# Performance work log

Hardware: AMD Instinct MI355X
Metric: run time of the kernel (lower is better)

The kernel has to match this reference:

```python
import jax, jax.numpy as jnp
import numpy as np

B, NNZ = 2048, 8
CAT_V, HVEC_V = 10000, 50000
SYN, SEM = 128, 256
HIDDEN, OUT = 1024, 10000


def setup_inputs() -> dict:
    key = jax.random.key(0)
    ks = jax.random.split(key, 12)
    d_onehot = jax.nn.one_hot(jax.random.randint(ks[0], (B,), 0, 7), 7, dtype=jnp.float32)
    cat_b_ix = jax.random.randint(ks[1], (B,), 0, CAT_V)
    hvb_ix = jax.random.randint(ks[2], (B, NNZ), 0, HVEC_V)
    hvf_ix = jax.random.randint(ks[3], (B, NNZ), 0, HVEC_V)
    hvb_top = jax.random.normal(ks[4], (B, SEM), dtype=jnp.float32)
    hvf_top = jax.random.normal(ks[5], (B, SEM), dtype=jnp.float32)
    cat_embeds = jax.random.normal(ks[6], (CAT_V, SYN), dtype=jnp.float32) * 0.02
    hvec_embeds = jax.random.normal(ks[7], (HVEC_V, SEM), dtype=jnp.float32) * 0.02
    in_dim = 7 + SYN + 2 * SEM
    W1 = jax.random.normal(ks[8], (HIDDEN, in_dim), dtype=jnp.float32) / np.sqrt(in_dim)
    b1 = jnp.zeros((HIDDEN,), dtype=jnp.float32)
    W2 = jax.random.normal(ks[9], (OUT, HIDDEN), dtype=jnp.float32) / np.sqrt(HIDDEN)
    b2 = jnp.zeros((OUT,), dtype=jnp.float32)
    return {"d_onehot": d_onehot, "cat_b_ix": cat_b_ix, "hvb_ix": hvb_ix,
            "hvf_ix": hvf_ix, "hvb_top": hvb_top, "hvf_top": hvf_top,
            "cat_embeds": cat_embeds, "hvec_embeds": hvec_embeds,
            "W1": W1, "b1": b1, "W2": W2, "b2": b2}


def _multi_hot(ix, vocab):
    # set-to-1 semantics: duplicates within a row still yield 1 (matches torch loop)
    rows = jnp.arange(ix.shape[0])[:, None]
    return jnp.zeros((ix.shape[0], vocab), dtype=jnp.float32).at[rows, ix].set(1.0)


def reference(d_onehot, cat_b_ix, hvb_ix, hvf_ix, hvb_top, hvf_top,
              cat_embeds, hvec_embeds, W1, b1, W2, b2):
    cat_b_embed = cat_embeds[cat_b_ix]                      # (B, SYN)
    hvb_mat = _multi_hot(hvb_ix, hvec_embeds.shape[0])      # (B, HVEC_V)
    hvf_mat = _multi_hot(hvf_ix, hvec_embeds.shape[0])
    hvb_embed = hvb_mat @ hvec_embeds + hvb_top             # (B, SEM)
    hvf_embed = hvf_mat @ hvec_embeds + hvf_top
    x = jnp.concatenate([cat_b_embed, hvb_embed, hvf_embed, d_onehot], axis=1)
    x = jax.nn.relu(x @ W1.T + b1)
    x = x @ W2.T + b2
    return jax.nn.log_softmax(x, axis=1)
```

## Files before the change

kernel.cpp:

```cpp
#include <hip/hip_runtime.h>

#define B_      2048
#define SYN     128
#define SEM     256
#define IN_DIM  647
#define K1      704
#define HIDDEN  1024
#define OUT_N   10000
#define NNZ     8

typedef __bf16 bf16x8 __attribute__((ext_vector_type(8)));
typedef float  f32x4  __attribute__((ext_vector_type(4)));
typedef __attribute__((address_space(3))) const unsigned short* lds_cp;

__device__ __forceinline__ unsigned short f2b(float v) {
    __bf16 b = (__bf16)v;
    return __builtin_bit_cast(unsigned short, b);
}

#define NB_W1 2816
#define NB_W2 5000
__global__ __launch_bounds__(256) void prep(
    const float* __restrict__ W1,  unsigned short* __restrict__ W1b,
    const float* __restrict__ W2,  unsigned short* __restrict__ W2b,
    const float* __restrict__ d_onehot,
    const int*   __restrict__ cat_ix,
    const int*   __restrict__ hvb_ix,
    const int*   __restrict__ hvf_ix,
    const float* __restrict__ hvb_top,
    const float* __restrict__ hvf_top,
    const float* __restrict__ cat_embeds,
    const float* __restrict__ hvec_embeds,
    unsigned short* __restrict__ xb)
{
    const int bb = blockIdx.x, t = threadIdx.x;
    if (bb < NB_W1) {
        int idx = bb * 256 + t;
        int r = idx / K1, c = idx - r * K1;
        W1b[idx] = f2b(c < IN_DIM ? W1[r * IN_DIM + c] : 0.f);
        return;
    }
    if (bb < NB_W1 + NB_W2) {
        size_t i = (size_t)(bb - NB_W1) * 256 + t;
        const float4* src = (const float4*)(W2 + i * 8);
        float4 a = src[0], b = src[1];
        ushort u[8] = { f2b(a.x), f2b(a.y), f2b(a.z), f2b(a.w),
                        f2b(b.x), f2b(b.y), f2b(b.z), f2b(b.w) };
        *(uint4*)(W2b + i * 8) = *(const uint4*)u;
        return;
    }
    const int b = bb - (NB_W1 + NB_W2);
    unsigned short* xrow = xb + (size_t)b * K1;
    if (t < SYN) {
        int c = cat_ix[b];
        xrow[t] = f2b(cat_embeds[(size_t)c * SYN + t]);
    }
    {
        int ix[NNZ];
        #pragma unroll
        for (int j = 0; j < NNZ; ++j) ix[j] = hvb_ix[b * NNZ + j];
        float s = hvb_top[(size_t)b * SEM + t];
        #pragma unroll
        for (int j = 0; j < NNZ; ++j) {
            bool dup = false;
            for (int k2 = 0; k2 < j; ++k2) dup = dup || (ix[j] == ix[k2]);
            if (!dup) s += hvec_embeds[(size_t)ix[j] * SEM + t];
        }
        xrow[SYN + t] = f2b(s);
    }
    {
        int ix[NNZ];
        #pragma unroll
        for (int j = 0; j < NNZ; ++j) ix[j] = hvf_ix[b * NNZ + j];
        float s = hvf_top[(size_t)b * SEM + t];
        #pragma unroll
        for (int j = 0; j < NNZ; ++j) {
            bool dup = false;
            for (int k2 = 0; k2 < j; ++k2) dup = dup || (ix[j] == ix[k2]);
            if (!dup) s += hvec_embeds[(size_t)ix[j] * SEM + t];
        }
        xrow[SYN + SEM + t] = f2b(s);
    }
    if (t < 7)       xrow[640 + t] = f2b(d_onehot[b * 7 + t]);
    else if (t < 64) xrow[640 + t] = 0;
}

template<int NI, int MODE>
__global__ __launch_bounds__(256) void gemm_rt(
    const unsigned short* __restrict__ A,
    const unsigned short* __restrict__ Bm,
    const float* __restrict__ bias,
    void* __restrict__ outp,
    int K, int nt, int ncols, int nbm1, int nm)
{
    constexpr int BN    = 32 * NI;
    constexpr int NB_CH = NI / 2;
    __shared__ __align__(16) unsigned short lds_a[4][128 * 32];
    __shared__ __align__(16) unsigned short lds_b[4][BN * 32];

    const int tid = threadIdx.x;
    const int wv = tid >> 6, ln = tid & 63;
    const int wr = wv >> 1, wc = wv & 1;
    const int lr = ln & 15, lh = ln >> 4;

    const int g   = gridDim.x;
    const int nw  = (blockIdx.x & 7) * (g >> 3) + (blockIdx.x >> 3);
    const int mt  = nw % nm, ntile = nw / nm;
    const int m0  = mt * 128, n0 = ntile * BN;

    const unsigned short* srcA[2];
    const unsigned short* srcB[NB_CH];
    #pragma unroll
    for (int i = 0; i < 2; ++i) {
        int c = tid + i * 256;
        int row = c >> 2, colL = (((c & 3) ^ ((c >> 3) & 3)) << 3);
        srcA[i] = A + (size_t)(m0 + row) * K + colL;
    }
    #pragma unroll
    for (int j = 0; j < NB_CH; ++j) {
        int c = tid + j * 256;
        int row = c >> 2, colL = (((c & 3) ^ ((c >> 3) & 3)) << 3);
        int gr = n0 + row; if (gr > nbm1) gr = nbm1;
        srcB[j] = Bm + (size_t)gr * K + colL;
    }

    auto stage = [&](int buf, int kt) {
        #pragma unroll
        for (int i = 0; i < 2; ++i)
            __builtin_amdgcn_global_load_lds(
                (__attribute__((address_space(1))) const void*)(srcA[i] + kt),
                (__attribute__((address_space(3))) void*)&lds_a[buf][(tid + i * 256) * 8], 16, 0, 0);
        #pragma unroll
        for (int j = 0; j < NB_CH; ++j)
            __builtin_amdgcn_global_load_lds(
                (__attribute__((address_space(1))) const void*)(srcB[j] + kt),
                (__attribute__((address_space(3))) void*)&lds_b[buf][(tid + j * 256) * 8], 16, 0, 0);
    };

    int a_off[4], b_off[NI];
    #pragma unroll
    for (int mi = 0; mi < 4; ++mi) {
        int row = wr * 64 + mi * 16 + lr;
        a_off[mi] = (row * 64 + lh * 16) ^ (((row >> 1) & 3) << 4);
    }
    #pragma unroll
    for (int ni = 0; ni < NI; ++ni) {
        int row = wc * 16 * NI + ni * 16 + lr;
        b_off[ni] = (row * 64 + lh * 16) ^ (((row >> 1) & 3) << 4);
    }

    f32x4 acc[4][NI];
    {
        f32x4 z = {0.f, 0.f, 0.f, 0.f};
        #pragma unroll
        for (int i = 0; i < 4; ++i)
            #pragma unroll
            for (int j = 0; j < NI; ++j) acc[i][j] = z;
    }

    auto frag_read = [&](bf16x8 (&af)[4], bf16x8 (&bfv)[NI], int buf) {
        lds_cp pa = (lds_cp)&lds_a[buf][0];
        lds_cp pb = (lds_cp)&lds_b[buf][0];
        #pragma unroll
        for (int mi = 0; mi < 4; ++mi) {
            unsigned ad = (unsigned)(unsigned long long)pa + a_off[mi];
            asm volatile("ds_read_b128 %0, %1" : "=v"(af[mi]) : "v"(ad));
        }
        #pragma unroll
        for (int ni = 0; ni < NI; ++ni) {
            unsigned ad = (unsigned)(unsigned long long)pb + b_off[ni];
            asm volatile("ds_read_b128 %0, %1" : "=v"(bfv[ni]) : "v"(ad));
        }
    };
    auto do_mfma = [&](bf16x8 (&af)[4], bf16x8 (&bfv)[NI]) {
        #pragma unroll
        for (int mi = 0; mi < 4; ++mi)
            #pragma unroll
            for (int ni = 0; ni < NI; ++ni)
                acc[mi][ni] = __builtin_amdgcn_mfma_f32_16x16x32_bf16(af[mi], bfv[ni], acc[mi][ni], 0, 0, 0);
    };
    auto do_part = [&](bf16x8 (&rA)[4], bf16x8 (&rB)[NI],
                       bf16x8 (&mA)[4], bf16x8 (&mB)[NI], int p) {
        frag_read(rA, rB, (p + 1) & 3);
        int tp = p + 3; if (tp > nt - 1) tp = nt - 1;
        stage((p + 3) & 3, tp * 32);
        if constexpr (NI == 4) asm volatile("s_waitcnt lgkmcnt(8)" ::: "memory");
        else                   asm volatile("s_waitcnt lgkmcnt(6)" ::: "memory");
        __builtin_amdgcn_sched_barrier(0);
        __builtin_amdgcn_s_setprio(1);
        do_mfma(mA, mB);
        __builtin_amdgcn_s_setprio(0);
        if constexpr (NI == 4) asm volatile("s_waitcnt vmcnt(4)" ::: "memory");
        else                   asm volatile("s_waitcnt vmcnt(3)" ::: "memory");
        __builtin_amdgcn_s_barrier();
    };

    stage(0, 0);
    stage(1, 32);
    stage(2, 64);
    if constexpr (NI == 4) asm volatile("s_waitcnt vmcnt(4)" ::: "memory");
    else                   asm volatile("s_waitcnt vmcnt(3)" ::: "memory");
    __builtin_amdgcn_s_barrier();

    bf16x8 afX[4], bfX[NI], afY[4], bfY[NI];
    frag_read(afX, bfX, 0);

    for (int t = 0; t < nt; t += 2) {
        do_part(afY, bfY, afX, bfX, t);
        do_part(afX, bfX, afY, bfY, t + 1);
    }

    #pragma unroll
    for (int mi = 0; mi < 4; ++mi) {
        int row = m0 + wr * 64 + mi * 16 + lh * 4;
        #pragma unroll
        for (int ni = 0; ni < NI; ++ni) {
            int col = n0 + wc * 16 * NI + ni * 16 + lr;
            if (col < ncols) {
                float bb = bias[col];
                if (MODE == 0) {
                    unsigned short* H = (unsigned short*)outp;
                    #pragma unroll
                    for (int r = 0; r < 4; ++r)
                        H[(size_t)(row + r) * ncols + col] = f2b(fmaxf(acc[mi][ni][r] + bb, 0.f));
                } else if (MODE == 1) {
                    unsigned short* H = (unsigned short*)outp;
                    #pragma unroll
                    for (int r = 0; r < 4; ++r)
                        H[(size_t)(row + r) * ncols + col] = f2b(acc[mi][ni][r] + bb);
                } else {
                    float* O = (float*)outp;
                    #pragma unroll
                    for (int r = 0; r < 4; ++r)
                        O[(size_t)(row + r) * ncols + col] = acc[mi][ni][r] + bb;
                }
            }
        }
    }
}

__global__ __launch_bounds__(256) void lsm_b(const unsigned short* __restrict__ lg,
                                             float* __restrict__ out) {
    __shared__ __align__(16) float rowbuf[OUT_N];
    __shared__ float red[8];
    const int t = threadIdx.x, wv = t >> 6, ln = t & 63;
    const unsigned short* l = lg + (size_t)blockIdx.x * OUT_N;
    float* o = out + (size_t)blockIdx.x * OUT_N;

    float mx = -3.4e38f;
    for (int i = t; i < OUT_N / 8; i += 256) {
        uint4 v = ((const uint4*)l)[i];
        float f[8];
        unsigned w[4] = {v.x, v.y, v.z, v.w};
        #pragma unroll
        for (int j = 0; j < 4; ++j) {
            f[2*j]   = __builtin_bit_cast(float, w[j] << 16);
            f[2*j+1] = __builtin_bit_cast(float, w[j] & 0xffff0000u);
        }
        #pragma unroll
        for (int j = 0; j < 8; ++j) {
            rowbuf[i * 8 + j] = f[j];
            mx = fmaxf(mx, f[j]);
        }
    }
    #pragma unroll
    for (int off = 32; off > 0; off >>= 1) mx = fmaxf(mx, __shfl_xor(mx, off, 64));
    if (ln == 0) red[wv] = mx;
    __syncthreads();
    float m4 = fmaxf(fmaxf(red[0], red[1]), fmaxf(red[2], red[3]));

    float s = 0.f;
    for (int i = t; i < OUT_N; i += 256) s += __expf(rowbuf[i] - m4);
    #pragma unroll
    for (int off = 32; off > 0; off >>= 1) s += __shfl_xor(s, off, 64);
    if (ln == 0) red[4 + wv] = s;
    __syncthreads();
    float lz = m4 + logf(red[4] + red[5] + red[6] + red[7]);

    for (int i = t; i < OUT_N / 4; i += 256) {
        float4 v = { rowbuf[i*4] - lz, rowbuf[i*4+1] - lz,
                     rowbuf[i*4+2] - lz, rowbuf[i*4+3] - lz };
        ((float4*)o)[i] = v;
    }
}

__global__ __launch_bounds__(256) void lsm_f(float* __restrict__ out) {
    __shared__ __align__(16) float rowbuf[OUT_N];
    __shared__ float red[8];
    const int t = threadIdx.x, wv = t >> 6, ln = t & 63;
    float* o = out + (size_t)blockIdx.x * OUT_N;

    float mx = -3.4e38f;
    for (int i = t; i < OUT_N / 4; i += 256) {
        float4 v = ((const float4*)o)[i];
        rowbuf[i*4] = v.x; rowbuf[i*4+1] = v.y; rowbuf[i*4+2] = v.z; rowbuf[i*4+3] = v.w;
        mx = fmaxf(fmaxf(mx, fmaxf(v.x, v.y)), fmaxf(v.z, v.w));
    }
    #pragma unroll
    for (int off = 32; off > 0; off >>= 1) mx = fmaxf(mx, __shfl_xor(mx, off, 64));
    if (ln == 0) red[wv] = mx;
    __syncthreads();
    float m4 = fmaxf(fmaxf(red[0], red[1]), fmaxf(red[2], red[3]));

    float s = 0.f;
    for (int i = t; i < OUT_N; i += 256) s += __expf(rowbuf[i] - m4);
    #pragma unroll
    for (int off = 32; off > 0; off >>= 1) s += __shfl_xor(s, off, 64);
    if (ln == 0) red[4 + wv] = s;
    __syncthreads();
    float lz = m4 + logf(red[4] + red[5] + red[6] + red[7]);

    for (int i = t; i < OUT_N / 4; i += 256) {
        float4 v = { rowbuf[i*4] - lz, rowbuf[i*4+1] - lz,
                     rowbuf[i*4+2] - lz, rowbuf[i*4+3] - lz };
        ((float4*)o)[i] = v;
    }
}

extern "C" void kernel_launch(void* const* d_in, const int* in_sizes, int n_in,
                              void* d_out, int out_size, void* d_ws, size_t ws_size,
                              hipStream_t stream) {
    const float* d_onehot    = (const float*)d_in[0];
    const int*   cat_ix      = (const int*)  d_in[1];
    const int*   hvb_ix      = (const int*)  d_in[2];
    const int*   hvf_ix      = (const int*)  d_in[3];
    const float* hvb_top     = (const float*)d_in[4];
    const float* hvf_top     = (const float*)d_in[5];
    const float* cat_embeds  = (const float*)d_in[6];
    const float* hvec_embeds = (const float*)d_in[7];
    const float* W1          = (const float*)d_in[8];
    const float* b1          = (const float*)d_in[9];
    const float* W2          = (const float*)d_in[10];
    const float* b2          = (const float*)d_in[11];
    float* out = (float*)d_out;

    unsigned short* xb  = (unsigned short*)d_ws;
    unsigned short* W1b = xb  + (size_t)B_ * K1;
    unsigned short* hB  = W1b + (size_t)HIDDEN * K1;
    unsigned short* W2b = hB  + (size_t)B_ * HIDDEN;
    unsigned short* lg  = W2b + (size_t)OUT_N * HIDDEN;
    const size_t need = ((size_t)B_*K1 + (size_t)HIDDEN*K1 + (size_t)B_*HIDDEN
                         + (size_t)OUT_N*HIDDEN + (size_t)B_*OUT_N) * 2;
    const bool bf16_logits = (ws_size >= need);

    prep<<<dim3(NB_W1 + NB_W2 + B_), dim3(256), 0, stream>>>(
        W1, W1b, W2, W2b, d_onehot, cat_ix, hvb_ix, hvf_ix,
        hvb_top, hvf_top, cat_embeds, hvec_embeds, xb);
    gemm_rt<2, 0><<<dim3(256), dim3(256), 0, stream>>>(
        xb, W1b, b1, (void*)hB, K1, K1 / 32, HIDDEN, HIDDEN - 1, 16);
    if (bf16_logits) {
        gemm_rt<4, 1><<<dim3(16 * 79), dim3(256), 0, stream>>>(
            hB, W2b, b2, (void*)lg, HIDDEN, HIDDEN / 32, OUT_N, OUT_N - 1, 16);
        lsm_b<<<dim3(B_), dim3(256), 0, stream>>>(lg, out);
    } else {
        gemm_rt<4, 2><<<dim3(16 * 79), dim3(256), 0, stream>>>(
            hB, W2b, b2, (void*)out, HIDDEN, HIDDEN / 32, OUT_N, OUT_N - 1, 16);
        lsm_f<<<dim3(B_), dim3(256), 0, stream>>>(out);
    }
}
```

Baseline: 116.3 us.

## Add 256x320-tile 4-stage pipelined GEMM for logits layer

Replaces the generic second GEMM (128-row tiles, 1264 blocks) with a dedicated 512-thread kernel using 256x320 tiles, giving exactly 256 blocks that cover 2048x10240 outputs. It keeps a 4-slot LDS ring filled with direct global-to-LDS loads, splits each k-step into two MFMA halves interleaved with staging, uses a swizzled LDS layout and raises wave priority around the MFMAs. The goal is to cut operand re-reads and tile-count overhead and to overlap loads with compute better. The cost is heavy register and LDS use (about 144KB LDS per block), and the last tile wastes columns past 10000.

```diff
diff --git a/kernel.cpp b/kernel.cpp
--- a/kernel.cpp
+++ b/kernel.cpp
@@ -223,17 +223,159 @@
                     #pragma unroll
                     for (int r = 0; r < 4; ++r)
                         H[(size_t)(row + r) * ncols + col] = f2b(fmaxf(acc[mi][ni][r] + bb, 0.f));
-                } else if (MODE == 1) {
-                    unsigned short* H = (unsigned short*)outp;
-                    #pragma unroll
-                    for (int r = 0; r < 4; ++r)
-                        H[(size_t)(row + r) * ncols + col] = f2b(acc[mi][ni][r] + bb);
                 } else {
                     float* O = (float*)outp;
                     #pragma unroll
                     for (int r = 0; r < 4; ++r)
                         O[(size_t)(row + r) * ncols + col] = acc[mi][ni][r] + bb;
                 }
+            }
+        }
+    }
+}
+
+__global__ __launch_bounds__(512, 2) void gemm2_320(
+    const unsigned short* __restrict__ A,
+    const unsigned short* __restrict__ Bm,
+    const float* __restrict__ bias,
+    unsigned short* __restrict__ H)
+{
+    __shared__ __align__(16) unsigned short lA[4][8192];
+    __shared__ __align__(16) unsigned short lB[4][10240];
+    const int tid = threadIdx.x;
+    const int wv = tid >> 6, ln = tid & 63;
+    const int wr = wv >> 2, wc = wv & 3;
+    const int lr = ln & 15, lh = ln >> 4;
+
+    const int nw = (blockIdx.x & 7) * 32 + (blockIdx.x >> 3);
+    const int m0 = (nw & 7) * 256;
+    const int n0 = (nw >> 3) * 320;
+
+    const unsigned short* srcA[2];
+    const unsigned short* srcB[2];
+    const unsigned short* srcB2;
+    #pragma unroll
+    for (int j = 0; j < 2; ++j) {
+        int c = j * 512 + tid;
+        int row = c >> 2, colL = (((c & 3) ^ ((c >> 3) & 3)) << 3);
+        srcA[j] = A + (size_t)(m0 + row) * HIDDEN + colL;
+        int gr = n0 + row; if (gr > OUT_N - 1) gr = OUT_N - 1;
+        srcB[j] = Bm + (size_t)gr * HIDDEN + colL;
+    }
+    const int c2 = 1024 + (wv & 3) * 64 + ln;
+    {
+        int row = c2 >> 2, colL = (((c2 & 3) ^ ((c2 >> 3) & 3)) << 3);
+        int gr = n0 + row; if (gr > OUT_N - 1) gr = OUT_N - 1;
+        srcB2 = Bm + (size_t)gr * HIDDEN + colL;
+    }
+
+    auto stageA = [&](int slot, int kt) {
+        #pragma unroll
+        for (int j = 0; j < 2; ++j)
+            __builtin_amdgcn_global_load_lds(
+                (__attribute__((address_space(1))) const void*)(srcA[j] + kt),
+                (__attribute__((address_space(3))) void*)&lA[slot][(j * 512 + tid) * 8], 16, 0, 0);
+    };
+    auto stageB = [&](int slot, int kt) {
+        #pragma unroll
+        for (int j = 0; j < 2; ++j)
+            __builtin_amdgcn_global_load_lds(
+                (__attribute__((address_space(1))) const void*)(srcB[j] + kt),
+                (__attribute__((address_space(3))) void*)&lB[slot][(j * 512 + tid) * 8], 16, 0, 0);
+        __builtin_amdgcn_global_load_lds(
+            (__attribute__((address_space(1))) const void*)(srcB2 + kt),
+            (__attribute__((address_space(3))) void*)&lB[slot][c2 * 8], 16, 0, 0);
+    };
+
+    int a_off[8], b_off[5];
+    #pragma unroll
+    for (int mi = 0; mi < 8; ++mi) {
+        int row = wr * 128 + mi * 16 + lr;
+        a_off[mi] = (row * 64 + lh * 16) ^ (((row >> 1) & 3) << 4);
+    }
+    #pragma unroll
+    for (int ni = 0; ni < 5; ++ni) {
+        int row = wc * 80 + ni * 16 + lr;
+        b_off[ni] = (row * 64 + lh * 16) ^ (((row >> 1) & 3) << 4);
+    }
+
+    f32x4 acc[8][5];
+    {
+        f32x4 z = {0.f, 0.f, 0.f, 0.f};
+        #pragma unroll
+        for (int i = 0; i < 8; ++i)
+            #pragma unroll
+            for (int j = 0; j < 5; ++j) acc[i][j] = z;
+    }
+
+    stageA(0, 0);  stageB(0, 0);
+    stageA(1, 32); stageB(1, 32);
+    stageA(2, 64); stageB(2, 64);
+    asm volatile("s_waitcnt vmcnt(10)" ::: "memory");
+    __builtin_amdgcn_s_barrier();
+
+    for (int t = 0; t < 32; ++t) {
+        const int slot = t & 3;
+        int tp = t + 3; if (tp > 31) tp = 31;
+        const int pslot = tp & 3;
+        lds_cp pA = (lds_cp)&lA[slot][0];
+        lds_cp pB = (lds_cp)&lB[slot][0];
+        bf16x8 af[4], bfv[5];
+
+        #pragma unroll
+        for (int ni = 0; ni < 5; ++ni) {
+            unsigned ad = (unsigned)(unsigned long long)pB + b_off[ni];
+            asm volatile("ds_read_b128 %0, %1" : "=v"(bfv[ni]) : "v"(ad));
+        }
+        #pragma unroll
+        for (int mi = 0; mi < 4; ++mi) {
+            unsigned ad = (unsigned)(unsigned long long)pA + a_off[mi];
+            asm volatile("ds_read_b128 %0, %1" : "=v"(af[mi]) : "v"(ad));
+        }
+        stageA(pslot, tp * 32);
+        __builtin_amdgcn_s_barrier();
+        asm volatile("s_waitcnt lgkmcnt(0)" ::: "memory");
+        __builtin_amdgcn_sched_barrier(0);
+        __builtin_amdgcn_s_setprio(1);
+        #pragma unroll
+        for (int mi = 0; mi < 4; ++mi)
+            #pragma unroll
+            for (int ni = 0; ni < 5; ++ni)
+                acc[mi][ni] = __builtin_amdgcn_mfma_f32_16x16x32_bf16(af[mi], bfv[ni], acc[mi][ni], 0, 0, 0);
+        __builtin_amdgcn_s_setprio(0);
+        __builtin_amdgcn_s_barrier();
+
+        #pragma unroll
+        for (int mi = 0; mi < 4; ++mi) {
+            unsigned ad = (unsigned)(unsigned long long)pA + a_off[4 + mi];
+            asm volatile("ds_read_b128 %0, %1" : "=v"(af[mi]) : "v"(ad));
+        }
+        stageB(pslot, tp * 32);
+        __builtin_amdgcn_s_barrier();
+        asm volatile("s_waitcnt lgkmcnt(0)" ::: "memory");
+        __builtin_amdgcn_sched_barrier(0);
+        __builtin_amdgcn_s_setprio(1);
+        #pragma unroll
+        for (int mi = 0; mi < 4; ++mi)
+            #pragma unroll
+            for (int ni = 0; ni < 5; ++ni)
+                acc[4 + mi][ni] = __builtin_amdgcn_mfma_f32_16x16x32_bf16(af[mi], bfv[ni], acc[4 + mi][ni], 0, 0, 0);
+        __builtin_amdgcn_s_setprio(0);
+        asm volatile("s_waitcnt vmcnt(10)" ::: "memory");
+        __builtin_amdgcn_s_barrier();
+    }
+
+    #pragma unroll
+    for (int mi = 0; mi < 8; ++mi) {
+        int row = m0 + wr * 128 + mi * 16 + lh * 4;
+        #pragma unroll
+        for (int ni = 0; ni < 5; ++ni) {
+            int col = n0 + wc * 80 + ni * 16 + lr;
+            if (col < OUT_N) {
+                float bb = bias[col];
+                #pragma unroll
+                for (int r = 0; r < 4; ++r)
+                    H[(size_t)(row + r) * OUT_N + col] = f2b(acc[mi][ni][r] + bb);
             }
         }
     }
@@ -349,8 +491,7 @@
     gemm_rt<2, 0><<<dim3(256), dim3(256), 0, stream>>>(
         xb, W1b, b1, (void*)hB, K1, K1 / 32, HIDDEN, HIDDEN - 1, 16);
     if (bf16_logits) {
-        gemm_rt<4, 1><<<dim3(16 * 79), dim3(256), 0, stream>>>(
-            hB, W2b, b2, (void*)lg, HIDDEN, HIDDEN / 32, OUT_N, OUT_N - 1, 16);
+        gemm2_320<<<dim3(256), dim3(512), 0, stream>>>(hB, W2b, b2, lg);
         lsm_b<<<dim3(B_), dim3(256), 0, stream>>>(lg, out);
     } else {
         gemm_rt<4, 2><<<dim3(16 * 79), dim3(256), 0, stream>>>(
```

After: 102.9 us. 11.5% less time.

## Widen output GEMM tile to 160 columns and simplify the prefetch pipeline

Applied to the files above, without the earlier changes.

The second GEMM moves from 128-wide to 160-wide N tiles (NI=5). The odd fifth B chunk is loaded by only half the threads, so the vmcnt waits are now per-wave. The main loop drops register-level fragment double buffering and the 3-deep prefetch in favour of a single-fragment loop with 2-deep LDS prefetch and a full lgkmcnt wait. Launch bounds now request 2 waves per SIMD, so occupancy rather than software pipelining is meant to hide latency. The grid of 1024 blocks includes a column of tiles lying fully beyond 10000 columns; those blocks do wasted work, and the simpler pipeline exposes LDS read latency.

```diff
diff --git a/kernel.cpp b/kernel.cpp
--- a/kernel.cpp
+++ b/kernel.cpp
@@ -85,16 +85,38 @@
     else if (t < 64) xrow[640 + t] = 0;
 }
 
+template<int NI> __device__ __forceinline__ void wait_vm(int wv) {
+    if constexpr (NI == 5) {
+        if (wv < 2) asm volatile("s_waitcnt vmcnt(5)" ::: "memory");
+        else        asm volatile("s_waitcnt vmcnt(4)" ::: "memory");
+    } else if constexpr (NI == 4) {
+        asm volatile("s_waitcnt vmcnt(4)" ::: "memory");
+    } else {
+        asm volatile("s_waitcnt vmcnt(3)" ::: "memory");
+    }
+}
+template<int NI> __device__ __forceinline__ void wait_vm2(int wv) {
+    if constexpr (NI == 5) {
+        if (wv < 2) asm volatile("s_waitcnt vmcnt(5)" ::: "memory");
+        else        asm volatile("s_waitcnt vmcnt(4)" ::: "memory");
+    } else if constexpr (NI == 4) {
+        asm volatile("s_waitcnt vmcnt(4)" ::: "memory");
+    } else {
+        asm volatile("s_waitcnt vmcnt(3)" ::: "memory");
+    }
+}
+
 template<int NI, int MODE>
-__global__ __launch_bounds__(256) void gemm_rt(
+__global__ __launch_bounds__(256, 2) void gemm_rt(
     const unsigned short* __restrict__ A,
     const unsigned short* __restrict__ Bm,
     const float* __restrict__ bias,
     void* __restrict__ outp,
     int K, int nt, int ncols, int nbm1, int nm)
 {
-    constexpr int BN    = 32 * NI;
-    constexpr int NB_CH = NI / 2;
+    constexpr int BN  = 32 * NI;
+    constexpr int BCH = NI / 2;
+    constexpr bool BX = (NI & 1);
     __shared__ __align__(16) unsigned short lds_a[4][128 * 32];
     __shared__ __align__(16) unsigned short lds_b[4][BN * 32];
 
@@ -109,7 +131,8 @@
     const int m0  = mt * 128, n0 = ntile * BN;
 
     const unsigned short* srcA[2];
-    const unsigned short* srcB[NB_CH];
+    const unsigned short* srcB[BCH];
+    const unsigned short* srcBx = nullptr;
     #pragma unroll
     for (int i = 0; i < 2; ++i) {
         int c = tid + i * 256;
@@ -117,12 +140,18 @@
         srcA[i] = A + (size_t)(m0 + row) * K + colL;
     }
     #pragma unroll
-    for (int j = 0; j < NB_CH; ++j) {
+    for (int j = 0; j < BCH; ++j) {
         int c = tid + j * 256;
         int row = c >> 2, colL = (((c & 3) ^ ((c >> 3) & 3)) << 3);
         int gr = n0 + row; if (gr > nbm1) gr = nbm1;
         srcB[j] = Bm + (size_t)gr * K + colL;
     }
+    if constexpr (BX) {
+        int c = tid + BCH * 256;
+        int row = c >> 2, colL = (((c & 3) ^ ((c >> 3) & 3)) << 3);
+        int gr = n0 + row; if (gr > nbm1) gr = nbm1;
+        srcBx = Bm + (size_t)gr * K + colL;
+    }
 
     auto stage = [&](int buf, int kt) {
         #pragma unroll
@@ -131,10 +160,16 @@
                 (__attribute__((address_space(1))) const void*)(srcA[i] + kt),
                 (__attribute__((address_space(3))) void*)&lds_a[buf][(tid + i * 256) * 8], 16, 0, 0);
         #pragma unroll
-        for (int j = 0; j < NB_CH; ++j)
+        for (int j = 0; j < BCH; ++j)
             __builtin_amdgcn_global_load_lds(
                 (__attribute__((address_space(1))) const void*)(srcB[j] + kt),
                 (__attribute__((address_space(3))) void*)&lds_b[buf][(tid + j * 256) * 8], 16, 0, 0);
+        if constexpr (BX) {
+            if (tid < 128)
+                __builtin_amdgcn_global_load_lds(
+                    (__attribute__((address_space(1))) const void*)(srcBx + kt),
+                    (__attribute__((address_space(3))) void*)&lds_b[buf][(tid + BCH * 256) * 8], 16, 0, 0);
+        }
     };
 
     int a_off[4], b_off[NI];
@@ -158,9 +193,18 @@
             for (int j = 0; j < NI; ++j) acc[i][j] = z;
     }
 
-    auto frag_read = [&](bf16x8 (&af)[4], bf16x8 (&bfv)[NI], int buf) {
-        lds_cp pa = (lds_cp)&lds_a[buf][0];
-        lds_cp pb = (lds_cp)&lds_b[buf][0];
+    stage(0, 0);
+    stage(1, 32);
+    wait_vm2<NI>(wv);
+    __builtin_amdgcn_s_barrier();
+
+    for (int t = 0; t < nt; ++t) {
+        const int slot = t & 3;
+        int tp = t + 2; if (tp > nt - 1) tp = nt - 1;
+
+        bf16x8 af[4], bfv[NI];
+        lds_cp pa = (lds_cp)&lds_a[slot][0];
+        lds_cp pb = (lds_cp)&lds_b[slot][0];
         #pragma unroll
         for (int mi = 0; mi < 4; ++mi) {
             unsigned ad = (unsigned)(unsigned long long)pa + a_off[mi];
@@ -171,43 +215,21 @@
             unsigned ad = (unsigned)(unsigned long long)pb + b_off[ni];
             asm volatile("ds_read_b128 %0, %1" : "=v"(bfv[ni]) : "v"(ad));
         }
-    };
-    auto do_mfma = [&](bf16x8 (&af)[4], bf16x8 (&bfv)[NI]) {
+
+        stage((t + 2) & 3, tp * 32);
+
+        asm volatile("s_waitcnt lgkmcnt(0)" ::: "memory");
+        __builtin_amdgcn_sched_barrier(0);
+        __builtin_amdgcn_s_setprio(1);
         #pragma unroll
         for (int mi = 0; mi < 4; ++mi)
             #pragma unroll
             for (int ni = 0; ni < NI; ++ni)
                 acc[mi][ni] = __builtin_amdgcn_mfma_f32_16x16x32_bf16(af[mi], bfv[ni], acc[mi][ni], 0, 0, 0);
-    };
-    auto do_part = [&](bf16x8 (&rA)[4], bf16x8 (&rB)[NI],
-                       bf16x8 (&mA)[4], bf16x8 (&mB)[NI], int p) {
-        frag_read(rA, rB, (p + 1) & 3);
-        int tp = p + 3; if (tp > nt - 1) tp = nt - 1;
-        stage((p + 3) & 3, tp * 32);
-        if constexpr (NI == 4) asm volatile("s_waitcnt lgkmcnt(8)" ::: "memory");
-        else                   asm volatile("s_waitcnt lgkmcnt(6)" ::: "memory");
-        __builtin_amdgcn_sched_barrier(0);
-        __builtin_amdgcn_s_setprio(1);
-        do_mfma(mA, mB);
         __builtin_amdgcn_s_setprio(0);
-        if constexpr (NI == 4) asm volatile("s_waitcnt vmcnt(4)" ::: "memory");
-        else                   asm volatile("s_waitcnt vmcnt(3)" ::: "memory");
+
+        wait_vm<NI>(wv);
         __builtin_amdgcn_s_barrier();
-    };
-
-    stage(0, 0);
-    stage(1, 32);
-    stage(2, 64);
-    if constexpr (NI == 4) asm volatile("s_waitcnt vmcnt(4)" ::: "memory");
-    else                   asm volatile("s_waitcnt vmcnt(3)" ::: "memory");
-    __builtin_amdgcn_s_barrier();
-
-    bf16x8 afX[4], bfX[NI], afY[4], bfY[NI];
-    frag_read(afX, bfX, 0);
-
-    for (int t = 0; t < nt; t += 2) {
-        do_part(afY, bfY, afX, bfX, t);
-        do_part(afX, bfX, afY, bfY, t + 1);
     }
 
     #pragma unroll
@@ -349,11 +371,11 @@
     gemm_rt<2, 0><<<dim3(256), dim3(256), 0, stream>>>(
         xb, W1b, b1, (void*)hB, K1, K1 / 32, HIDDEN, HIDDEN - 1, 16);
     if (bf16_logits) {
-        gemm_rt<4, 1><<<dim3(16 * 79), dim3(256), 0, stream>>>(
+        gemm_rt<5, 1><<<dim3(1024), dim3(256), 0, stream>>>(
             hB, W2b, b2, (void*)lg, HIDDEN, HIDDEN / 32, OUT_N, OUT_N - 1, 16);
         lsm_b<<<dim3(B_), dim3(256), 0, stream>>>(lg, out);
     } else {
-        gemm_rt<4, 2><<<dim3(16 * 79), dim3(256), 0, stream>>>(
+        gemm_rt<5, 2><<<dim3(1024), dim3(256), 0, stream>>>(
             hB, W2b, b2, (void*)out, HIDDEN, HIDDEN / 32, OUT_N, OUT_N - 1, 16);
         lsm_f<<<dim3(B_), dim3(256), 0, stream>>>(out);
     }
```

Result: faster. 111.1 us (-4.4%).
